# Performance work log

Measured on AMD Instinct MI355X. Metric: run time of the kernel, lower is better.

The kernel has to match this reference:

```python
import jax, jax.numpy as jnp
import numpy as np

B, S, D = 4, 2048, 1024

def setup_inputs() -> dict:
    key = jax.random.key(0)
    k0, k1, k2, k3, k4, k5 = jax.random.split(key, 6)
    scale = 1.0 / np.sqrt(D)
    return {
        "input_seq_embs": jax.random.normal(k0, (B, S, D), dtype=jnp.float32),
        "W_Q": jax.random.normal(k1, (D, D), dtype=jnp.float32) * scale,
        "W_K": jax.random.normal(k2, (D, D), dtype=jnp.float32) * scale,
        "W_V": jax.random.normal(k3, (D, D), dtype=jnp.float32) * scale,
        "W_O": jax.random.normal(k4, (D, D), dtype=jnp.float32) * scale,
        "b_O": jax.random.normal(k5, (D,), dtype=jnp.float32) * 0.01,
    }

def reference(input_seq_embs, W_Q, W_K, W_V, W_O, b_O):
    # torch nn.Linear: y = x @ W.T
    Q = jnp.einsum('bsd,ed->bse', input_seq_embs, W_Q)
    K = jnp.einsum('bsd,ed->bse', input_seq_embs, W_K)
    V = jnp.einsum('bsd,ed->bse', input_seq_embs, W_V)
    # NOTE: no 1/sqrt(d) scaling in the original module
    A = jnp.einsum('bqd,bkd->bqk', Q, K)  # [B,S,S]
    # log(tril(ones)) == 0 on/below diagonal, -inf above
    causal = jnp.tril(jnp.ones((S, S), dtype=bool))
    A = jnp.where(causal[None, :, :], A, -jnp.inf)
    A = jax.nn.softmax(A, axis=-1)
    # dropout layers are identity in eval mode
    out = jnp.einsum('bqk,bkd->bqd', A, V)
    out = jnp.einsum('bsd,ed->bse', out, W_O) + b_O
    return out
```

## Files before the change

### kernel.cpp

```cpp
#include <hip/hip_runtime.h>
#include <cstdint>

typedef _Float16 f16x8 __attribute__((ext_vector_type(8)));
typedef _Float16 f16x4 __attribute__((ext_vector_type(4)));
typedef float    f32x4 __attribute__((ext_vector_type(4)));

#define AS1 __attribute__((address_space(1)))
#define AS3 __attribute__((address_space(3)))

__device__ __forceinline__ void load16_lds(const void* g, void* l) {
  __builtin_amdgcn_global_load_lds((AS1 void*)g, (AS3 void*)l, 16, 0, 0);
}

#define GEMM_PROLOGUE(Ab, lda, Bb, ldb)                                   \
  __shared__ _Float16 lA[2 * 128 * 32];                                   \
  __shared__ _Float16 lB[2 * 128 * 32];                                   \
  int tid = threadIdx.x;                                                  \
  int r0 = tid >> 2;                                                      \
  int c0 = (tid & 3) * 8;                                                 \
  const _Float16* ga0 = Ab + (long long)r0 * lda + c0;                    \
  const _Float16* ga1 = Ab + (long long)(r0 + 64) * lda + c0;             \
  const _Float16* gb0 = Bb + (long long)r0 * ldb + c0;                    \
  const _Float16* gb1 = Bb + (long long)(r0 + 64) * ldb + c0;             \
  _Float16* la0 = lA + tid * 8;                                           \
  _Float16* la1 = lA + 2048 + tid * 8;                                    \
  _Float16* la2 = lA + 4096 + tid * 8;                                    \
  _Float16* la3 = lA + 6144 + tid * 8;                                    \
  _Float16* lb0 = lB + tid * 8;                                           \
  _Float16* lb1 = lB + 2048 + tid * 8;                                    \
  _Float16* lb2 = lB + 4096 + tid * 8;                                    \
  _Float16* lb3 = lB + 6144 + tid * 8;                                    \
  f32x4 acc[4][4] = {};                                                   \
  int lane = tid & 63;                                                    \
  int wv = tid >> 6;                                                      \
  int wm = (wv & 1) * 64, wn = (wv >> 1) * 64;                            \
  int l16 = lane & 15, quad = lane >> 4;                                  \
  const _Float16* raBase = lA + (wm + l16) * 32 + quad * 8;               \
  const _Float16* rbBase = lB + (wn + l16) * 32 + quad * 8;

#define GEMM_KLOOP(lda, ldb, KLEN, SWAP)                                  \
  for (int kb = 0; kb < (KLEN); kb += 64) {                               \
    __syncthreads();                                                      \
    load16_lds(ga0, la0);                                                 \
    load16_lds(ga1, la1);                                                 \
    load16_lds(ga0 + 32, la2);                                            \
    load16_lds(ga1 + 32, la3);                                            \
    load16_lds(gb0, lb0);                                                 \
    load16_lds(gb1, lb1);                                                 \
    load16_lds(gb0 + 32, lb2);                                            \
    load16_lds(gb1 + 32, lb3);                                            \
    ga0 += 64; ga1 += 64; gb0 += 64; gb1 += 64;                           \
    __syncthreads();                                                      \
    _Pragma("unroll")                                                     \
    for (int s = 0; s < 2; s++) {                                         \
      f16x8 af[4], bfr[4];                                                \
      _Pragma("unroll")                                                   \
      for (int i = 0; i < 4; i++)                                         \
        af[i] = *(const f16x8*)(raBase + s * 4096 + i * 512);             \
      _Pragma("unroll")                                                   \
      for (int j = 0; j < 4; j++)                                         \
        bfr[j] = *(const f16x8*)(rbBase + s * 4096 + j * 512);            \
      _Pragma("unroll")                                                   \
      for (int i = 0; i < 4; i++)                                         \
        _Pragma("unroll")                                                 \
        for (int j = 0; j < 4; j++)                                       \
          acc[i][j] = (SWAP)                                              \
            ? __builtin_amdgcn_mfma_f32_16x16x32_f16(bfr[j], af[i], acc[i][j], 0, 0, 0) \
            : __builtin_amdgcn_mfma_f32_16x16x32_f16(af[i], bfr[j], acc[i][j], 0, 0, 0);\
    }                                                                     \
  }

__global__ __launch_bounds__(256) void cvt_all(
    const float* __restrict__ x, const float* __restrict__ wq,
    const float* __restrict__ wk, const float* __restrict__ wv,
    const float* __restrict__ wo,
    _Float16* __restrict__ xh, _Float16* __restrict__ wcat,
    _Float16* __restrict__ woh) {
  long long g = (long long)blockIdx.x * 256 + threadIdx.x;
  const float* in; _Float16* out; long long idx;
  if (g < 2097152)      { in = x;  out = xh;             idx = g; }
  else if (g < 2359296) { in = wq; out = wcat;           idx = g - 2097152; }
  else if (g < 2621440) { in = wk; out = wcat + 1048576; idx = g - 2359296; }
  else if (g < 2883584) { in = wv; out = wcat + 2097152; idx = g - 2621440; }
  else                  { in = wo; out = woh;            idx = g - 2883584; }
  float4 v = ((const float4*)in)[idx];
  f16x4 o;
  o[0] = (_Float16)v.x; o[1] = (_Float16)v.y; o[2] = (_Float16)v.z; o[3] = (_Float16)v.w;
  ((f16x4*)out)[idx] = o;
}

#define VMW(NLIT) asm volatile("s_waitcnt vmcnt(" #NLIT ")" ::: "memory")

#define A0R 0
#define B0R 16384
#define A1R 32768
#define B1R 49152

#define SGA(reg, u, kc) load16_lds(pA + (u) * 65536 + (kc), shm + (reg) + (u) * 4096 + tid * 8)
#define SGB(reg, u, kc) load16_lds(pB + (u) * 65536 + (kc), shm + (reg) + (u) * 4096 + tid * 8)

#define QPH(ABASE, BBASE, MQ, SWAP, STAGES, WAITS)                         \
  {                                                                        \
    if ((MQ) == 0) {                                                       \
      _Pragma("unroll")                                                    \
      for (int nf = 0; nf < 4; nf++) {                                     \
        int o = (BBASE) + rbw + nf * 1024;                                 \
        bf[nf][0] = *(const f16x8*)(shm + o);                              \
        bf[nf][1] = *(const f16x8*)(shm + (o ^ 32));                       \
      }                                                                    \
    }                                                                      \
    f16x8 af[2][2];                                                        \
    _Pragma("unroll")                                                      \
    for (int mi = 0; mi < 2; mi++) {                                       \
      int o = (ABASE) + raw + ((MQ) * 2 + mi) * 1024;                      \
      af[mi][0] = *(const f16x8*)(shm + o);                                \
      af[mi][1] = *(const f16x8*)(shm + (o ^ 32));                         \
    }                                                                      \
    STAGES                                                                 \
    WAITS                                                                  \
    __builtin_amdgcn_sched_barrier(0);                                     \
    __builtin_amdgcn_s_barrier();                                          \
    asm volatile("s_waitcnt lgkmcnt(0)" ::: "memory");                     \
    __builtin_amdgcn_sched_barrier(0);                                     \
    __builtin_amdgcn_s_setprio(1);                                         \
    _Pragma("unroll")                                                      \
    for (int ks = 0; ks < 2; ks++)                                         \
      _Pragma("unroll")                                                    \
      for (int mi = 0; mi < 2; mi++)                                       \
        _Pragma("unroll")                                                  \
        for (int nf = 0; nf < 4; nf++)                                     \
          acc[(MQ) * 2 + mi][nf] = (SWAP)                                  \
            ? __builtin_amdgcn_mfma_f32_16x16x32_f16(bf[nf][ks], af[mi][ks], acc[(MQ) * 2 + mi][nf], 0, 0, 0) \
            : __builtin_amdgcn_mfma_f32_16x16x32_f16(af[mi][ks], bf[nf][ks], acc[(MQ) * 2 + mi][nf], 0, 0, 0); \
    __builtin_amdgcn_s_setprio(0);                                         \
    __builtin_amdgcn_sched_barrier(0);                                     \
    __builtin_amdgcn_s_barrier();                                          \
  }

#define QKV_SETUP(APTR, BPTR)                                              \
  __shared__ _Float16 shm[65536];                                          \
  int tid = threadIdx.x;                                                   \
  const _Float16* pA = (APTR) + (long long)(tid >> 3) * 1024 +             \
                       ((tid & 7) ^ ((tid >> 3) & 7)) * 8;                 \
  const _Float16* pB = (BPTR) + (long long)(tid >> 3) * 1024 +             \
                       ((tid & 7) ^ ((tid >> 3) & 7)) * 8;                 \
  int lane = tid & 63, wv = tid >> 6;                                      \
  int wr = wv & 1, wc = wv >> 1;                                           \
  int l16 = lane & 15, quad = lane >> 4;                                   \
  int cswz = (quad ^ (l16 & 7)) * 8;                                       \
  int raw = (wr * 128 + l16) * 64 + cswz;                                  \
  int rbw = (wc * 64 + l16) * 64 + cswz;                                   \
  f32x4 acc[8][4] = {};

#define QKV_PRO()                                                          \
  SGB(B0R, 0, 0); SGB(B0R, 1, 0); SGB(B0R, 2, 0); SGB(B0R, 3, 0);          \
  SGA(A0R, 0, 0); SGA(A0R, 1, 0); SGA(A0R, 2, 0); SGA(A0R, 3, 0);          \
  SGB(B1R, 0, 64); SGB(B1R, 1, 64); SGB(B1R, 2, 64); SGB(B1R, 3, 64);      \
  SGA(A1R, 0, 64); SGA(A1R, 2, 64);                                        \
  VMW(6);                                                                  \
  __builtin_amdgcn_s_barrier();

#define QKV_MAIN(SWAP)                                                     \
  _Pragma("unroll 1")                                                      \
  for (int it = 0; it < 7; ++it) {                                         \
    int kb = it * 128;                                                     \
    f16x8 bf[4][2];                                                        \
    QPH(A0R, B0R, 0, SWAP, { SGA(A1R, 1, kb + 64);  SGA(A1R, 3, kb + 64); }, {})  \
    QPH(A0R, B0R, 1, SWAP, { SGB(B0R, 0, kb + 128); SGB(B0R, 1, kb + 128); }, {}) \
    QPH(A0R, B0R, 2, SWAP, { SGB(B0R, 2, kb + 128); SGB(B0R, 3, kb + 128); }, {}) \
    QPH(A0R, B0R, 3, SWAP, { SGA(A0R, 0, kb + 128); SGA(A0R, 2, kb + 128); }, { VMW(6); }) \
    QPH(A1R, B1R, 0, SWAP, { SGA(A0R, 1, kb + 128); SGA(A0R, 3, kb + 128); }, {}) \
    QPH(A1R, B1R, 1, SWAP, { SGB(B1R, 0, kb + 192); SGB(B1R, 1, kb + 192); }, {}) \
    QPH(A1R, B1R, 2, SWAP, { SGB(B1R, 2, kb + 192); SGB(B1R, 3, kb + 192); }, {}) \
    QPH(A1R, B1R, 3, SWAP, { SGA(A1R, 0, kb + 192); SGA(A1R, 2, kb + 192); }, { VMW(6); }) \
  }                                                                        \
  {                                                                        \
    f16x8 bf[4][2];                                                        \
    QPH(A0R, B0R, 0, SWAP, { SGA(A1R, 1, 960); SGA(A1R, 3, 960); }, {})    \
    QPH(A0R, B0R, 1, SWAP, {}, {})                                         \
    QPH(A0R, B0R, 2, SWAP, {}, {})                                         \
    QPH(A0R, B0R, 3, SWAP, {}, { VMW(0); })                                \
    QPH(A1R, B1R, 0, SWAP, {}, {})                                         \
    QPH(A1R, B1R, 1, SWAP, {}, {})                                         \
    QPH(A1R, B1R, 2, SWAP, {}, {})                                         \
    QPH(A1R, B1R, 3, SWAP, {}, {})                                         \
  }

__global__ __launch_bounds__(512, 2) void qkv_qk(
    const _Float16* __restrict__ A, const _Float16* __restrict__ B,
    _Float16* __restrict__ Qh, _Float16* __restrict__ Kh) {
  int bid = blockIdx.x;
  int swz = (bid & 7) * 32 + (bid >> 3);
  int by = swz >> 3, bx = swz & 7;
  QKV_SETUP(A + (long long)by * 262144, B + (long long)bx * 262144)
  QKV_PRO()
  QKV_MAIN(1)
  _Float16* C = (bx < 4) ? Qh : Kh;
  int m0 = by * 256 + wr * 128 + l16;
  int n0 = (bx & 3) * 256 + wc * 64 + quad * 4;
  #pragma unroll
  for (int i = 0; i < 8; i++)
    #pragma unroll
    for (int j = 0; j < 4; j++) {
      f16x4 pk;
      #pragma unroll
      for (int r = 0; r < 4; r++) pk[r] = (_Float16)acc[i][j][r];
      *(f16x4*)(C + (long long)(m0 + i * 16) * 1024 + (n0 + j * 16)) = pk;
    }
}

__global__ __launch_bounds__(512, 2) void qkv_v(
    const _Float16* __restrict__ A, const _Float16* __restrict__ B,
    _Float16* __restrict__ Vt) {
  int bid = blockIdx.x;
  int swz = (bid & 7) * 16 + (bid >> 3);
  int by = swz >> 2, bx = swz & 3;
  QKV_SETUP(A + (long long)by * 262144, B + (long long)(bx + 8) * 262144)
  QKV_PRO()
  QKV_MAIN(0)
  int d0 = bx * 256 + wc * 64 + l16;
  int mg0 = by * 256 + wr * 128 + quad * 4;
  #pragma unroll
  for (int i = 0; i < 8; i++) {
    long long mg = mg0 + i * 16;
    long long b = mg >> 11;
    long long s = mg & 2047;
    #pragma unroll
    for (int j = 0; j < 4; j++) {
      f16x4 pk;
      #pragma unroll
      for (int r = 0; r < 4; r++) pk[r] = (_Float16)acc[i][j][r];
      *(f16x4*)(Vt + (b << 21) + (long long)(d0 + j * 16) * 2048 + s) = pk;
    }
  }
}

__global__ __launch_bounds__(256) void scores_gemm(
    const _Float16* __restrict__ Qh, const _Float16* __restrict__ Kh,
    _Float16* __restrict__ S, float2* __restrict__ stats) {
  int L = blockIdx.x;
  int xcd = L & 7;
  int bz = xcd >> 1;
  int t = (L >> 3) + (xcd & 1) * 136;
  int g = (int)((__builtin_sqrtf(4.0f * t + 1.0f) - 1.0f) * 0.5f);
  while ((g + 1) * (g + 2) <= t) g++;
  while (g * (g + 1) > t) g--;
  int rem = t - g * (g + 1);
  int by = 2 * g + (rem > g ? 1 : 0);
  int bxt = (rem > g) ? rem - (g + 1) : rem;
  bool diag = (bxt == g);

  const _Float16* Ab = Qh + (long long)bz * 2097152 + (long long)by * 64 * 1024;
  const _Float16* Bb = Kh + (long long)bz * 2097152 + (long long)bxt * 128 * 1024;

  __shared__ _Float16 lA[2 * 64 * 32];
  __shared__ _Float16 lB[2 * 128 * 32];
  __shared__ float redM[4][64];
  __shared__ float redL[4][64];

  int tid = threadIdx.x;
  int r0 = tid >> 2;
  int c0 = (tid & 3) * 8;
  const _Float16* ga0 = Ab + (long long)r0 * 1024 + c0;
  const _Float16* gb0 = Bb + (long long)r0 * 1024 + c0;
  const _Float16* gb1 = Bb + (long long)(r0 + 64) * 1024 + c0;
  _Float16* la0 = lA + tid * 8;
  _Float16* la1 = lA + 2048 + tid * 8;
  _Float16* lb0 = lB + tid * 8;
  _Float16* lb1 = lB + 2048 + tid * 8;
  _Float16* lb2 = lB + 4096 + tid * 8;
  _Float16* lb3 = lB + 6144 + tid * 8;

  f32x4 acc[4][2] = {};
  int lane = tid & 63;
  int wv = tid >> 6;
  int wn = wv * 32;
  int l16 = lane & 15, quad = lane >> 4;
  const _Float16* raBase = lA + l16 * 32 + quad * 8;
  const _Float16* rbBase = lB + (wn + l16) * 32 + quad * 8;

  for (int kb = 0; kb < 1024; kb += 64) {
    __syncthreads();
    load16_lds(ga0, la0);
    load16_lds(ga0 + 32, la1);
    load16_lds(gb0, lb0);
    load16_lds(gb1, lb1);
    load16_lds(gb0 + 32, lb2);
    load16_lds(gb1 + 32, lb3);
    ga0 += 64; gb0 += 64; gb1 += 64;
    __syncthreads();
    #pragma unroll
    for (int s = 0; s < 2; s++) {
      f16x8 af[4], bfr[2];
      #pragma unroll
      for (int i = 0; i < 4; i++) af[i] = *(const f16x8*)(raBase + s * 2048 + i * 512);
      #pragma unroll
      for (int j = 0; j < 2; j++) bfr[j] = *(const f16x8*)(rbBase + s * 4096 + j * 512);
      #pragma unroll
      for (int i = 0; i < 4; i++)
        #pragma unroll
        for (int j = 0; j < 2; j++)
          acc[i][j] = __builtin_amdgcn_mfma_f32_16x16x32_f16(bfr[j], af[i], acc[i][j], 0, 0, 0);
    }
  }

  int rowBase = by * 64;
  int colBase = bxt * 128;

  float mloc[4];
  #pragma unroll
  for (int i = 0; i < 4; i++) {
    int grow = rowBase + 16 * i + l16;
    float mx = -3.0e38f;
    #pragma unroll
    for (int j = 0; j < 2; j++)
      #pragma unroll
      for (int r = 0; r < 4; r++) {
        bool ok = !diag || (colBase + wn + 16 * j + quad * 4 + r <= grow);
        mx = ok ? fmaxf(mx, acc[i][j][r]) : mx;
      }
    mx = fmaxf(mx, __shfl_xor(mx, 16));
    mx = fmaxf(mx, __shfl_xor(mx, 32));
    mloc[i] = mx;
  }
  if (quad == 0) {
    #pragma unroll
    for (int i = 0; i < 4; i++) redM[wv][16 * i + l16] = mloc[i];
  }
  __syncthreads();
  float mfin[4];
  #pragma unroll
  for (int i = 0; i < 4; i++) {
    int rl = 16 * i + l16;
    mfin[i] = fmaxf(fmaxf(redM[0][rl], redM[1][rl]), fmaxf(redM[2][rl], redM[3][rl]));
  }

  float lloc[4];
  #pragma unroll
  for (int i = 0; i < 4; i++) {
    int grow = rowBase + 16 * i + l16;
    float sum = 0.f;
    #pragma unroll
    for (int j = 0; j < 2; j++)
      #pragma unroll
      for (int r = 0; r < 4; r++) {
        bool ok = !diag || (colBase + wn + 16 * j + quad * 4 + r <= grow);
        float e = __expf(acc[i][j][r] - mfin[i]);
        sum += ok ? e : 0.f;
      }
    sum += __shfl_xor(sum, 16);
    sum += __shfl_xor(sum, 32);
    lloc[i] = sum;
  }
  if (quad == 0) {
    #pragma unroll
    for (int i = 0; i < 4; i++) redL[wv][16 * i + l16] = lloc[i];
  }
  __syncthreads();
  if (wv == 0 && quad == 0) {
    #pragma unroll
    for (int i = 0; i < 4; i++) {
      int rl = 16 * i + l16;
      float lt = redL[0][rl] + redL[1][rl] + redL[2][rl] + redL[3][rl];
      stats[((long long)bz * 2048 + rowBase + rl) * 16 + bxt] =
          make_float2(mfin[i], lt);
    }
  }

  _Float16* Sb = S + (long long)bz * 4194304;
  #pragma unroll
  for (int i = 0; i < 4; i++) {
    long long grow = rowBase + 16 * i + l16;
    #pragma unroll
    for (int j = 0; j < 2; j++) {
      f16x4 u;
      #pragma unroll
      for (int r = 0; r < 4; r++) u[r] = (_Float16)(acc[i][j][r] - mfin[i]);
      *(f16x4*)(Sb + grow * 2048 + (colBase + wn + 16 * j + quad * 4)) = u;
    }
  }
}

__global__ __launch_bounds__(256) void normalize_p(_Float16* __restrict__ S,
                                                   const float2* __restrict__ stats) {
  int g = blockIdx.x;
  int bz = g >> 11, row = g & 2047;
  int nt = (row >> 7) + 1;
  _Float16* srow = S + ((long long)bz * 2048 + row) * 2048;
  const float2* st = stats + ((long long)bz * 2048 + row) * 16;
  __shared__ float sh_invl;
  __shared__ float shd[16];
  int t = threadIdx.x;
  if (t < 16) {
    float2 p = (t < nt) ? st[t] : make_float2(-3.0e38f, 0.f);
    float m = p.x;
    #pragma unroll
    for (int d = 1; d < 16; d <<= 1) m = fmaxf(m, __shfl_xor(m, d));
    float term = p.y * __expf(p.x - m);
    #pragma unroll
    for (int d = 1; d < 16; d <<= 1) term += __shfl_xor(term, d);
    shd[t] = p.x - m;
    if (t == 0) sh_invl = 1.0f / term;
  }
  __syncthreads();
  float invl = sh_invl;
  int Lp = nt << 7;
  for (int c = t; (c << 3) < Lp; c += 256) {
    float dt = shd[c >> 4];
    f16x8 v = ((f16x8*)srow)[c];
    f16x8 o;
    int col0 = c << 3;
    #pragma unroll
    for (int e = 0; e < 8; e++) {
      float u = (float)v[e];
      float pe = __expf(u + dt) * invl;
      o[e] = (col0 + e <= row) ? (_Float16)pe : (_Float16)0.f;
    }
    ((f16x8*)srow)[c] = o;
  }
}

__global__ __launch_bounds__(256) void pv_splitk(
    const _Float16* __restrict__ P,
    const _Float16* __restrict__ Vt,
    float* __restrict__ P0, float* __restrict__ P1,
    _Float16* __restrict__ Oh) {
  int bid = blockIdx.x;
  int xcd = bid & 7;
  int bz = xcd >> 1;
  int idx = bid >> 3;
  int cy = idx >> 2;
  int bx = (xcd & 1) * 4 + (idx & 3);
  int by, c;
  if (cy < 8) { by = cy; c = 0; }
  else { int q = cy - 8; by = 8 + (q >> 1); c = q & 1; }
  int kmax = (by + 1) * 128;
  int k0 = c * 1024;
  int klen = min(kmax, k0 + 1024) - k0;

  const _Float16* Ab = P + (long long)bz * 4194304LL + (long long)by * 128 * 2048 + k0;
  const _Float16* Bb = Vt + (long long)bz * 2097152LL + (long long)bx * 128 * 2048 + k0;
  GEMM_PROLOGUE(Ab, 2048, Bb, 2048)
  GEMM_KLOOP(2048, 2048, klen, true)

  int m0 = by * 128 + wm + l16;
  int n0 = bx * 128 + wn + quad * 4;

  if (c == 0 && by < 8) {
    _Float16* C = Oh + (long long)bz * 2097152LL;
    #pragma unroll
    for (int i = 0; i < 4; i++)
      #pragma unroll
      for (int j = 0; j < 4; j++) {
        f16x4 pk;
        #pragma unroll
        for (int r = 0; r < 4; r++) pk[r] = (_Float16)acc[i][j][r];
        *(f16x4*)(C + (long long)(m0 + i * 16) * 1024 + (n0 + j * 16)) = pk;
      }
  } else if (c == 0) {
    float* C = P0 + (long long)bz * 2097152LL;
    #pragma unroll
    for (int i = 0; i < 4; i++)
      #pragma unroll
      for (int j = 0; j < 4; j++)
        *(f32x4*)(C + (long long)(m0 + i * 16) * 1024 + (n0 + j * 16)) = acc[i][j];
  } else {
    float* C = P1 + (long long)bz * 1048576LL;
    int mr = m0 - 1024;
    #pragma unroll
    for (int i = 0; i < 4; i++)
      #pragma unroll
      for (int j = 0; j < 4; j++)
        *(f32x4*)(C + (long long)(mr + i * 16) * 1024 + (n0 + j * 16)) = acc[i][j];
  }
}

__global__ __launch_bounds__(256) void pv_reduce(const float* __restrict__ P0,
                                                 const float* __restrict__ P1,
                                                 _Float16* __restrict__ Oh) {
  int i = blockIdx.x * 256 + threadIdx.x;
  if (i >= 1048576) return;
  int f4 = i;
  int bz = f4 >> 18;
  int loc = f4 & 262143;
  long long p0i = (long long)bz * 524288 + 262144 + loc;
  float4 v = ((const float4*)P0)[p0i];
  float4 w = ((const float4*)P1)[f4];
  v.x += w.x; v.y += w.y; v.z += w.z; v.w += w.w;
  f16x4 o;
  o[0] = (_Float16)v.x; o[1] = (_Float16)v.y; o[2] = (_Float16)v.z; o[3] = (_Float16)v.w;
  ((f16x4*)Oh)[p0i] = o;
}

__global__ __launch_bounds__(256) void oproj_gemm(
    const _Float16* __restrict__ A, const _Float16* __restrict__ B,
    float* __restrict__ C, const float* __restrict__ bias) {
  int bx = blockIdx.x, by = blockIdx.y;
  const _Float16* Ab = A + (long long)by * 128 * 1024;
  const _Float16* Bb = B + (long long)bx * 128 * 1024;
  GEMM_PROLOGUE(Ab, 1024, Bb, 1024)
  GEMM_KLOOP(1024, 1024, 1024, true)

  int m0 = by * 128 + wm + l16;
  int n0 = bx * 128 + wn + quad * 4;
  #pragma unroll
  for (int j = 0; j < 4; j++) {
    float4 b4 = *(const float4*)(bias + n0 + j * 16);
    #pragma unroll
    for (int i = 0; i < 4; i++) {
      f32x4 v = acc[i][j];
      v[0] += b4.x; v[1] += b4.y; v[2] += b4.z; v[3] += b4.w;
      *(f32x4*)(C + (long long)(m0 + i * 16) * 1024 + (n0 + j * 16)) = v;
    }
  }
}


extern "C" void kernel_launch(void* const* d_in, const int* in_sizes, int n_in,
                              void* d_out, int out_size, void* d_ws, size_t ws_size,
                              hipStream_t stream) {
  const float* x  = (const float*)d_in[0];
  const float* Wq = (const float*)d_in[1];
  const float* Wk = (const float*)d_in[2];
  const float* Wv = (const float*)d_in[3];
  const float* Wo = (const float*)d_in[4];
  const float* bO = (const float*)d_in[5];

  char* ws = (char*)d_ws;
  _Float16* xh   = (_Float16*)(ws + 0);
  _Float16* Wcat = (_Float16*)(ws + 16777216);
  _Float16* Woh  = (_Float16*)(ws + 23068672);
  _Float16* Qh   = (_Float16*)(ws + 25165824);
  _Float16* Kh   = (_Float16*)(ws + 41943040);
  _Float16* Vt   = (_Float16*)(ws + 58720256);
  _Float16* Oh   = (_Float16*)(ws + 75497472);
  _Float16* Sb   = (_Float16*)(ws + 92274688);
  float2*   stats= (float2*)  (ws + 125829120);
  float*    P0   = (float*)   (ws + 25165824);
  float*    P1   = (float*)   (ws + 0);

  dim3 blk(256);

  cvt_all<<<12288, blk, 0, stream>>>(x, Wq, Wk, Wv, Wo, xh, Wcat, Woh);

  qkv_qk<<<256, dim3(512), 0, stream>>>(xh, Wcat, Qh, Kh);
  qkv_v<<<128, dim3(512), 0, stream>>>(xh, Wcat, Vt);

  scores_gemm<<<1088, blk, 0, stream>>>(Qh, Kh, Sb, stats);

  normalize_p<<<8192, blk, 0, stream>>>(Sb, stats);

  pv_splitk<<<768, blk, 0, stream>>>(Sb, Vt, P0, P1, Oh);
  pv_reduce<<<4096, blk, 0, stream>>>(P0, P1, Oh);

  oproj_gemm<<<dim3(8, 64, 1), blk, 0, stream>>>(Oh, Woh, (float*)d_out, bO);
}
```

Baseline: 281.8 us.

## Use 128x128 tiles for causal scores GEMM via shared GEMM macros

The scores kernel moves from 64x128 tiles (1088 blocks) to 128x128 lower-triangular tiles (544 blocks), reusing the shared GEMM prologue and k-loop macros. Each wave now covers a 64x64 quadrant, so the row max and row sum reductions combine two waves per row half instead of four. The larger tile roughly halves global and LDS traffic per output element and raises MFMA work per load. The cost is fewer blocks to fill the GPU, more diagonal-tile waste, and higher register pressure from the 4x4 accumulator.

```diff
diff --git a/kernel.cpp b/kernel.cpp
--- a/kernel.cpp
+++ b/kernel.cpp
@@ -239,81 +239,33 @@
     const _Float16* __restrict__ Qh, const _Float16* __restrict__ Kh,
     _Float16* __restrict__ S, float2* __restrict__ stats) {
   int L = blockIdx.x;
-  int xcd = L & 7;
-  int bz = xcd >> 1;
-  int t = (L >> 3) + (xcd & 1) * 136;
-  int g = (int)((__builtin_sqrtf(4.0f * t + 1.0f) - 1.0f) * 0.5f);
-  while ((g + 1) * (g + 2) <= t) g++;
-  while (g * (g + 1) > t) g--;
-  int rem = t - g * (g + 1);
-  int by = 2 * g + (rem > g ? 1 : 0);
-  int bxt = (rem > g) ? rem - (g + 1) : rem;
-  bool diag = (bxt == g);
-
-  const _Float16* Ab = Qh + (long long)bz * 2097152 + (long long)by * 64 * 1024;
-  const _Float16* Bb = Kh + (long long)bz * 2097152 + (long long)bxt * 128 * 1024;
-
-  __shared__ _Float16 lA[2 * 64 * 32];
-  __shared__ _Float16 lB[2 * 128 * 32];
+  int swz = (L & 7) * 68 + (L >> 3);
+  int bz = swz / 136;
+  int t = swz % 136;
+  int g = (int)((__builtin_sqrtf(8.0f * t + 1.0f) - 1.0f) * 0.5f);
+  while ((g + 1) * (g + 2) / 2 <= t) g++;
+  while (g * (g + 1) / 2 > t) g--;
+  int by = g;
+  int bx = t - g * (g + 1) / 2;
+  bool diag = (bx == by);
+
+  const _Float16* Ab = Qh + (long long)bz * 2097152 + (long long)by * 128 * 1024;
+  const _Float16* Bb = Kh + (long long)bz * 2097152 + (long long)bx * 128 * 1024;
+  GEMM_PROLOGUE(Ab, 1024, Bb, 1024)
   __shared__ float redM[4][64];
   __shared__ float redL[4][64];
-
-  int tid = threadIdx.x;
-  int r0 = tid >> 2;
-  int c0 = (tid & 3) * 8;
-  const _Float16* ga0 = Ab + (long long)r0 * 1024 + c0;
-  const _Float16* gb0 = Bb + (long long)r0 * 1024 + c0;
-  const _Float16* gb1 = Bb + (long long)(r0 + 64) * 1024 + c0;
-  _Float16* la0 = lA + tid * 8;
-  _Float16* la1 = lA + 2048 + tid * 8;
-  _Float16* lb0 = lB + tid * 8;
-  _Float16* lb1 = lB + 2048 + tid * 8;
-  _Float16* lb2 = lB + 4096 + tid * 8;
-  _Float16* lb3 = lB + 6144 + tid * 8;
-
-  f32x4 acc[4][2] = {};
-  int lane = tid & 63;
-  int wv = tid >> 6;
-  int wn = wv * 32;
-  int l16 = lane & 15, quad = lane >> 4;
-  const _Float16* raBase = lA + l16 * 32 + quad * 8;
-  const _Float16* rbBase = lB + (wn + l16) * 32 + quad * 8;
-
-  for (int kb = 0; kb < 1024; kb += 64) {
-    __syncthreads();
-    load16_lds(ga0, la0);
-    load16_lds(ga0 + 32, la1);
-    load16_lds(gb0, lb0);
-    load16_lds(gb1, lb1);
-    load16_lds(gb0 + 32, lb2);
-    load16_lds(gb1 + 32, lb3);
-    ga0 += 64; gb0 += 64; gb1 += 64;
-    __syncthreads();
-    #pragma unroll
-    for (int s = 0; s < 2; s++) {
-      f16x8 af[4], bfr[2];
-      #pragma unroll
-      for (int i = 0; i < 4; i++) af[i] = *(const f16x8*)(raBase + s * 2048 + i * 512);
-      #pragma unroll
-      for (int j = 0; j < 2; j++) bfr[j] = *(const f16x8*)(rbBase + s * 4096 + j * 512);
-      #pragma unroll
-      for (int i = 0; i < 4; i++)
-        #pragma unroll
-        for (int j = 0; j < 2; j++)
-          acc[i][j] = __builtin_amdgcn_mfma_f32_16x16x32_f16(bfr[j], af[i], acc[i][j], 0, 0, 0);
-    }
-  }
-
-  int rowBase = by * 64;
-  int colBase = bxt * 128;
+  GEMM_KLOOP(1024, 1024, 1024, true)
+
+  int rowBase = by * 128;
+  int colBase = bx * 128;
 
   float mloc[4];
   #pragma unroll
   for (int i = 0; i < 4; i++) {
-    int grow = rowBase + 16 * i + l16;
+    int grow = rowBase + wm + 16 * i + l16;
     float mx = -3.0e38f;
     #pragma unroll
-    for (int j = 0; j < 2; j++)
+    for (int j = 0; j < 4; j++)
       #pragma unroll
       for (int r = 0; r < 4; r++) {
         bool ok = !diag || (colBase + wn + 16 * j + quad * 4 + r <= grow);
@@ -328,20 +280,21 @@
     for (int i = 0; i < 4; i++) redM[wv][16 * i + l16] = mloc[i];
   }
   __syncthreads();
+  int par = wv & 1;
   float mfin[4];
   #pragma unroll
   for (int i = 0; i < 4; i++) {
     int rl = 16 * i + l16;
-    mfin[i] = fmaxf(fmaxf(redM[0][rl], redM[1][rl]), fmaxf(redM[2][rl], redM[3][rl]));
+    mfin[i] = fmaxf(redM[par][rl], redM[par + 2][rl]);
   }
 
   float lloc[4];
   #pragma unroll
   for (int i = 0; i < 4; i++) {
-    int grow = rowBase + 16 * i + l16;
+    int grow = rowBase + wm + 16 * i + l16;
     float sum = 0.f;
     #pragma unroll
-    for (int j = 0; j < 2; j++)
+    for (int j = 0; j < 4; j++)
       #pragma unroll
       for (int r = 0; r < 4; r++) {
         bool ok = !diag || (colBase + wn + 16 * j + quad * 4 + r <= grow);
@@ -357,12 +310,12 @@
     for (int i = 0; i < 4; i++) redL[wv][16 * i + l16] = lloc[i];
   }
   __syncthreads();
-  if (wv == 0 && quad == 0) {
+  if (wv < 2 && quad == 0) {
     #pragma unroll
     for (int i = 0; i < 4; i++) {
       int rl = 16 * i + l16;
-      float lt = redL[0][rl] + redL[1][rl] + redL[2][rl] + redL[3][rl];
-      stats[((long long)bz * 2048 + rowBase + rl) * 16 + bxt] =
+      float lt = redL[wv][rl] + redL[wv + 2][rl];
+      stats[((long long)bz * 2048 + rowBase + wv * 64 + rl) * 16 + bx] =
           make_float2(mfin[i], lt);
     }
   }
@@ -370,9 +323,9 @@
   _Float16* Sb = S + (long long)bz * 4194304;
   #pragma unroll
   for (int i = 0; i < 4; i++) {
-    long long grow = rowBase + 16 * i + l16;
-    #pragma unroll
-    for (int j = 0; j < 2; j++) {
+    long long grow = rowBase + wm + 16 * i + l16;
+    #pragma unroll
+    for (int j = 0; j < 4; j++) {
       f16x4 u;
       #pragma unroll
       for (int r = 0; r < 4; r++) u[r] = (_Float16)(acc[i][j][r] - mfin[i]);
@@ -546,7 +499,7 @@
   qkv_qk<<<256, dim3(512), 0, stream>>>(xh, Wcat, Qh, Kh);
   qkv_v<<<128, dim3(512), 0, stream>>>(xh, Wcat, Vt);
 
-  scores_gemm<<<1088, blk, 0, stream>>>(Qh, Kh, Sb, stats);
+  scores_gemm<<<544, blk, 0, stream>>>(Qh, Kh, Sb, stats);
 
   normalize_p<<<8192, blk, 0, stream>>>(Sb, stats);
 
```

After: 289.1 us. 2.6% more time.
